# Kernel tuning notes

Measured on AMD Instinct MI355X. Metric: run time of the kernel, lower is better.

The kernel has to match this reference:

```python
import jax, jax.numpy as jnp
import numpy as np

EPS = 1e-8  # torch CosineSimilarity eps


def _neg_indices(N):
    # boolean mask removing diag and the +/-N diagonals, then per-row column
    # indices of the surviving (negative) entries: shape (2N, 2N-2)
    two_n = 2 * N
    mask = ~(np.eye(two_n, dtype=bool)
             | np.eye(two_n, k=N, dtype=bool)
             | np.eye(two_n, k=-N, dtype=bool))
    rows, cols = np.nonzero(mask)  # row-major order matches torch bool indexing
    return cols.reshape(two_n, two_n - 2)


def setup_inputs() -> dict:
    key = jax.random.key(0)
    k1, k2 = jax.random.split(key)
    B, D = 4096, 128
    return {
        "zis": jax.random.normal(k1, (B, D), dtype=jnp.float32),
        "zjs": jax.random.normal(k2, (B, D), dtype=jnp.float32),
    }


def reference(zis, zjs):
    N = zis.shape[0]
    temperature = 0.5
    reps = jnp.concatenate([zjs, zis], axis=0)            # (2N, D)
    norms = jnp.maximum(jnp.linalg.norm(reps, axis=-1, keepdims=True), EPS)
    r = reps / norms
    sim = r @ r.T                                         # (2N, 2N) cosine sims
    l_pos = jnp.diagonal(sim, offset=N)                   # (N,)
    r_pos = jnp.diagonal(sim, offset=-N)                  # (N,)
    positives = jnp.concatenate([l_pos, r_pos])[:, None]  # (2N, 1)
    neg_idx = jnp.asarray(_neg_indices(N))                # (2N, 2N-2) static
    negatives = jnp.take_along_axis(sim, neg_idx, axis=1) # (2N, 2N-2)
    logits = jnp.concatenate([positives, negatives], axis=1) / temperature
    # CrossEntropy with labels all 0, reduction='sum'
    loss = -jnp.sum(jax.nn.log_softmax(logits, axis=-1)[:, 0])
    return loss / (2 * N)
```

## Files before the change

kernel.cpp:

```cpp
#include <hip/hip_runtime.h>
#include <hip/hip_bf16.h>
#include <stdint.h>

typedef __attribute__((ext_vector_type(8))) short bf16x8;
typedef __attribute__((ext_vector_type(4))) float f32x4;

#define TWO_N 8192
#define NHALF 4096
#define DIM   128

#define SQRT_C 1.69864361f
#define LN2    0.69314718055994531f

__device__ __forceinline__ unsigned int f2bf(float f) {
  unsigned int u = __float_as_uint(f);
  u += 0x7FFFu + ((u >> 16) & 1u);
  return u >> 16;
}

__global__ __launch_bounds__(256) void norm_kernel(
    const float* __restrict__ zis, const float* __restrict__ zjs,
    unsigned int* __restrict__ rbf ) {
  const int wave = threadIdx.x >> 6;
  const int lane = threadIdx.x & 63;
  const int row = blockIdx.x * 4 + wave;
  const float* src = (row < NHALF) ? (zjs + (size_t)row * DIM)
                                   : (zis + (size_t)(row - NHALF) * DIM);
  float2 v = ((const float2*)src)[lane];
  float ss = v.x * v.x + v.y * v.y;
#pragma unroll
  for (int m = 1; m <= 32; m <<= 1) ss += __shfl_xor(ss, m);
  const float scale = SQRT_C / fmaxf(sqrtf(ss), 1e-8f);
  const unsigned int lo = f2bf(v.x * scale);
  const unsigned int hi = f2bf(v.y * scale);
  rbf[(size_t)row * (DIM / 2) + lane] = lo | (hi << 16);
}

__global__ __launch_bounds__(256)
__attribute__((amdgpu_waves_per_eu(2, 2)))
void simloss_kernel(
    const char* __restrict__ rbytes,
    float* __restrict__ pos,
    float* __restrict__ s_part) {
  const int t = threadIdx.x;
  const int rb = blockIdx.x >> 3;
  const int cs = blockIdx.x & 7;
  const int RB = rb * 128;
  const int CS = cs * 1024;
  const int wave = t >> 6;
  const int lane = t & 63;
  const int wr = wave >> 1, wc = wave & 1;
  const int lrow = lane >> 4, lcol = lane & 15;

  bf16x8 a_reg[4][4];
#pragma unroll
  for (int ks = 0; ks < 4; ++ks)
#pragma unroll
    for (int m = 0; m < 4; ++m)
      a_reg[ks][m] = *(const bf16x8*)(
          rbytes + (size_t)(RB + wr * 64 + m * 16 + lcol) * 256 +
          ks * 64 + lrow * 16);

  float srun[4][4];
#pragma unroll
  for (int m = 0; m < 4; ++m)
#pragma unroll
    for (int r = 0; r < 4; ++r) srun[m][r] = 0.0f;

  const char* bptr = rbytes + (size_t)(CS + wc * 64 + lcol) * 256 + lrow * 16;

#pragma unroll 1
  for (int ct = 0; ct < 8; ++ct) {
    const int CB = CS + ct * 128;

    bf16x8 bfr[4][4];
#pragma unroll
    for (int n = 0; n < 4; ++n)
#pragma unroll
      for (int ks = 0; ks < 4; ++ks)
        bfr[ks][n] = *(const bf16x8*)(bptr + n * 4096 + ks * 64);

    f32x4 acc[4][4];
#pragma unroll
    for (int m = 0; m < 4; ++m)
#pragma unroll
      for (int n = 0; n < 4; ++n) acc[m][n] = (f32x4){0.f, 0.f, 0.f, 0.f};

#pragma unroll
    for (int ks = 0; ks < 4; ++ks)
#pragma unroll
      for (int m = 0; m < 4; ++m)
#pragma unroll
        for (int n = 0; n < 4; ++n)
          acc[m][n] = __builtin_amdgcn_mfma_f32_16x16x32_bf16(
              a_reg[ks][m], bfr[ks][n], acc[m][n], 0, 0, 0);

#pragma unroll
    for (int m = 0; m < 4; ++m) {
      const int R0 = RB + wr * 64 + m * 16;
#pragma unroll
      for (int n = 0; n < 4; ++n) {
        const int C0 = CB + wc * 64 + n * 16;
        const bool hasDiag = (C0 == R0);
        const bool hasPartner = (C0 == (R0 ^ 4096));
#pragma unroll
        for (int r = 0; r < 4; ++r) {
          const float v = acc[m][n][r];
          float e = __builtin_amdgcn_exp2f(v);
          const bool mine = (lcol == lrow * 4 + r);
          if (hasPartner && mine) pos[R0 + lrow * 4 + r] = v;
          if (hasDiag && mine) e = 0.0f;
          srun[m][r] += e;
        }
      }
    }
    bptr += 32768;
  }

#pragma unroll
  for (int m = 0; m < 4; ++m)
#pragma unroll
    for (int r = 0; r < 4; ++r) {
      float s = srun[m][r];
      s += __shfl_xor(s, 1);
      s += __shfl_xor(s, 2);
      s += __shfl_xor(s, 4);
      s += __shfl_xor(s, 8);
      if (lcol == 0)
        s_part[(size_t)(cs * 2 + wc) * TWO_N +
               (RB + wr * 64 + m * 16 + lrow * 4 + r)] = s;
    }
}

__global__ __launch_bounds__(256) void reduce1_kernel(
    const float* __restrict__ pos, const float* __restrict__ s_part,
    float* __restrict__ partial) {
  const int t = threadIdx.x;
  const int row = blockIdx.x * 256 + t;
  float s = 0.0f;
#pragma unroll
  for (int q = 0; q < 16; ++q) s += s_part[(size_t)q * TWO_N + row];
  float local = (__log2f(s) - pos[row]) * LN2;
#pragma unroll
  for (int m = 1; m <= 32; m <<= 1) local += __shfl_xor(local, m);
  __shared__ float wsum[4];
  if ((t & 63) == 0) wsum[t >> 6] = local;
  __syncthreads();
  if (t == 0) partial[blockIdx.x] = wsum[0] + wsum[1] + wsum[2] + wsum[3];
}

__global__ __launch_bounds__(64) void reduce2_kernel(
    const float* __restrict__ partial, float* __restrict__ out) {
  float v = (threadIdx.x < 32) ? partial[threadIdx.x] : 0.0f;
#pragma unroll
  for (int m = 1; m <= 32; m <<= 1) v += __shfl_xor(v, m);
  if (threadIdx.x == 0) out[0] = v * (1.0f / TWO_N);
}

extern "C" void kernel_launch(void* const* d_in, const int* in_sizes, int n_in,
                              void* d_out, int out_size, void* d_ws, size_t ws_size,
                              hipStream_t stream) {
  const float* zis = (const float*)d_in[0];
  const float* zjs = (const float*)d_in[1];
  char* ws = (char*)d_ws;
  unsigned int* rbf = (unsigned int*)ws;
  float* pos = (float*)(ws + 2u * 1024 * 1024);
  float* s_part = (float*)(ws + 2u * 1024 * 1024 + 32 * 1024);
  float* partial = (float*)(ws + 2u * 1024 * 1024 + 544 * 1024);

  norm_kernel<<<TWO_N / 4, 256, 0, stream>>>(zis, zjs, rbf);
  simloss_kernel<<<512, 256, 0, stream>>>((const char*)rbf, pos, s_part);
  reduce1_kernel<<<TWO_N / 256, 256, 0, stream>>>(pos, s_part, partial);
  reduce2_kernel<<<1, 64, 0, stream>>>(partial, (float*)d_out);
}
```

Before: 99.75 us.

## Stage B tiles through double-buffered LDS with async global-to-LDS loads

After: 86.72 us. -13.1%, faster.

```diff
diff --git a/kernel.cpp b/kernel.cpp
--- a/kernel.cpp
+++ b/kernel.cpp
@@ -36,12 +36,30 @@
   rbf[(size_t)row * (DIM / 2) + lane] = lo | (hi << 16);
 }
 
+#define GLL16(SRC, DST) __builtin_amdgcn_global_load_lds( \
+    (__attribute__((address_space(1))) void*)(SRC),       \
+    (__attribute__((address_space(3))) void*)(DST), 16, 0, 0)
+
+#define STAGE128(ROWBASE, DST) do {                                        \
+  _Pragma("unroll")                                                        \
+  for (int i_ = 0; i_ < 8; ++i_) {                                         \
+    const int L_ = (i_ * 256 + t) * 16;                                    \
+    const int row_ = L_ >> 8;                                              \
+    const int cb_ = L_ & 255;                                              \
+    GLL16(rbytes + (size_t)((ROWBASE) + row_) * 256 +                      \
+              (cb_ ^ ((row_ & 7) << 4)),                                   \
+          (DST) + L_);                                                     \
+  }                                                                        \
+} while (0)
+
 __global__ __launch_bounds__(256)
 __attribute__((amdgpu_waves_per_eu(2, 2)))
 void simloss_kernel(
     const char* __restrict__ rbytes,
     float* __restrict__ pos,
     float* __restrict__ s_part) {
+  __shared__ char Bb0[32768];
+  __shared__ char Bb1[32768];
   const int t = threadIdx.x;
   const int rb = blockIdx.x >> 3;
   const int cs = blockIdx.x & 7;
@@ -61,24 +79,32 @@
           rbytes + (size_t)(RB + wr * 64 + m * 16 + lcol) * 256 +
           ks * 64 + lrow * 16);
 
+  STAGE128(CS, Bb0);
+  STAGE128(CS + 128, Bb1);
+
   float srun[4][4];
 #pragma unroll
   for (int m = 0; m < 4; ++m)
 #pragma unroll
     for (int r = 0; r < 4; ++r) srun[m][r] = 0.0f;
-
-  const char* bptr = rbytes + (size_t)(CS + wc * 64 + lcol) * 256 + lrow * 16;
 
 #pragma unroll 1
   for (int ct = 0; ct < 8; ++ct) {
-    const int CB = CS + ct * 128;
-
+    if (ct < 7) asm volatile("s_waitcnt vmcnt(8)" ::: "memory");
+    else        asm volatile("s_waitcnt vmcnt(0)" ::: "memory");
+    __builtin_amdgcn_s_barrier();
+    __builtin_amdgcn_sched_barrier(0);
+
+    const char* curB = (ct & 1) ? Bb1 : Bb0;
     bf16x8 bfr[4][4];
 #pragma unroll
     for (int n = 0; n < 4; ++n)
 #pragma unroll
-      for (int ks = 0; ks < 4; ++ks)
-        bfr[ks][n] = *(const bf16x8*)(bptr + n * 4096 + ks * 64);
+      for (int ks = 0; ks < 4; ++ks) {
+        const int row = wc * 64 + n * 16 + lcol;
+        const int kb = ks * 64 + lrow * 16;
+        bfr[ks][n] = *(const bf16x8*)(curB + row * 256 + (kb ^ ((row & 7) << 4)));
+      }
 
     f32x4 acc[4][4];
 #pragma unroll
@@ -95,6 +121,12 @@
           acc[m][n] = __builtin_amdgcn_mfma_f32_16x16x32_bf16(
               a_reg[ks][m], bfr[ks][n], acc[m][n], 0, 0, 0);
 
+    __builtin_amdgcn_sched_barrier(0);
+    __builtin_amdgcn_s_barrier();
+    __builtin_amdgcn_sched_barrier(0);
+    if (ct < 6) STAGE128(CS + (ct + 2) * 128, (char*)((ct & 1) ? Bb1 : Bb0));
+
+    const int CB = CS + ct * 128;
 #pragma unroll
     for (int m = 0; m < 4; ++m) {
       const int R0 = RB + wr * 64 + m * 16;
@@ -114,7 +146,6 @@
         }
       }
     }
-    bptr += 32768;
   }
 
 #pragma unroll
```
